# Optimization experiments

Measured on AMD Instinct MI355X. Metric: run time of the kernel, lower is better.

The kernel has to match this reference:

```python
import jax, jax.numpy as jnp
import numpy as np

B, Q, E, NH, L, P = 8, 1024, 256, 8, 4, 4
DH = E // NH
SHAPES = np.array([[128, 128], [64, 64], [32, 32], [16, 16]], dtype=np.int64)
STARTS = np.concatenate([[0], np.cumsum(SHAPES.prod(1))[:-1]]).astype(np.int64)
S_TOTAL = int(SHAPES.prod(1).sum())
EPS = 1e-5


def setup_inputs() -> dict:
    key = jax.random.key(0)
    ks = iter(jax.random.split(key, 40))
    def rn(shp, s=0.02):
        return jax.random.normal(next(ks), shp, jnp.float32) * s
    return {
        "tgt": rn((B, Q, E), 1.0),
        "query_pos": rn((B, Q, E), 1.0),
        "reference_points": jax.random.uniform(next(ks), (B, Q, L, 2), jnp.float32),
        "src": rn((B, S_TOTAL, E), 1.0),
        "spatial_shapes": jnp.asarray(SHAPES),
        "level_start_index": jnp.asarray(STARTS),
        "in_proj_w": rn((3 * E, E)), "in_proj_b": jnp.zeros((3 * E,), jnp.float32),
        "out_proj_w": rn((E, E)), "out_proj_b": jnp.zeros((E,), jnp.float32),
        "norm1_g": jnp.ones((E,), jnp.float32), "norm1_b": jnp.zeros((E,), jnp.float32),
        "off_w": rn((NH * L * P * 2, E)), "off_b": rn((NH * L * P * 2,), 0.5),
        "aw_w": rn((NH * L * P, E)), "aw_b": jnp.zeros((NH * L * P,), jnp.float32),
        "vp_w": rn((E, E)), "vp_b": jnp.zeros((E,), jnp.float32),
        "op_w": rn((E, E)), "op_b": jnp.zeros((E,), jnp.float32),
        "norm2_g": jnp.ones((E,), jnp.float32), "norm2_b": jnp.zeros((E,), jnp.float32),
        "w1": rn((4 * E, E)), "b1": jnp.zeros((4 * E,), jnp.float32),
        "w2": rn((E, 4 * E)), "b2": jnp.zeros((E,), jnp.float32),
        "norm3_g": jnp.ones((E,), jnp.float32), "norm3_b": jnp.zeros((E,), jnp.float32),
    }


def _ln(x, g, b):
    mu = x.mean(-1, keepdims=True)
    var = ((x - mu) ** 2).mean(-1, keepdims=True)
    return (x - mu) * jax.lax.rsqrt(var + EPS) * g + b


def _bilinear(v, loc, Hl, Wl):
    # v: [B,NH,S_l,DH], loc in [0,1]: [B,NH,Q,P,2] -> [B,NH,Q,P,DH]
    # matches torch grid_sample(align_corners=False, padding='zeros')
    x = loc[..., 0] * Wl - 0.5
    y = loc[..., 1] * Hl - 0.5
    x0 = jnp.floor(x)
    y0 = jnp.floor(y)
    wx = (x - x0)[..., None]
    wy = (y - y0)[..., None]
    def g(yi, xi):
        valid = ((xi >= 0) & (xi <= Wl - 1) & (yi >= 0) & (yi <= Hl - 1)).astype(v.dtype)
        idx = (jnp.clip(yi, 0, Hl - 1) * Wl + jnp.clip(xi, 0, Wl - 1)).astype(jnp.int32)
        out = jnp.take_along_axis(v, idx.reshape(B, NH, Q * P, 1), axis=2)
        return out.reshape(B, NH, Q, P, DH) * valid[..., None]
    v00 = g(y0, x0); v01 = g(y0, x0 + 1.0)
    v10 = g(y0 + 1.0, x0); v11 = g(y0 + 1.0, x0 + 1.0)
    return (v00 * (1 - wy) * (1 - wx) + v01 * (1 - wy) * wx
            + v10 * wy * (1 - wx) + v11 * wy * wx)


def _forward(tgt, query_pos, reference_points, src,
             in_proj_w, in_proj_b, out_proj_w, out_proj_b, norm1_g, norm1_b,
             off_w, off_b, aw_w, aw_b, vp_w, vp_b, op_w, op_b,
             norm2_g, norm2_b, w1, b1, w2, b2, norm3_g, norm3_b,
             spatial_shapes, level_start_index):
    shp = np.asarray(spatial_shapes)
    starts = np.asarray(level_start_index)
    # ---- self-attention (q = k = tgt + pos, v = tgt) ----
    qk = tgt + query_pos
    wq, wk, wv = jnp.split(in_proj_w, 3, axis=0)
    bq, bk, bv = jnp.split(in_proj_b, 3, axis=0)
    q = (qk @ wq.T + bq).reshape(B, Q, NH, DH)
    k = (qk @ wk.T + bk).reshape(B, Q, NH, DH)
    v = (tgt @ wv.T + bv).reshape(B, Q, NH, DH)
    scores = jnp.einsum("bqhd,bkhd->bhqk", q, k) / jnp.sqrt(jnp.float32(DH))
    attn = jax.nn.softmax(scores, axis=-1)
    ctx = jnp.einsum("bhqk,bkhd->bqhd", attn, v).reshape(B, Q, E)
    tgt = _ln(tgt + (ctx @ out_proj_w.T + out_proj_b), norm1_g, norm1_b)
    # ---- MSDA cross-attention ----
    query = tgt + query_pos
    value = (src @ vp_w.T + vp_b).reshape(B, S_TOTAL, NH, DH).transpose(0, 2, 1, 3)  # [B,NH,S,DH]
    off = (query @ off_w.T + off_b).reshape(B, Q, NH, L, P, 2)
    aw = jax.nn.softmax((query @ aw_w.T + aw_b).reshape(B, Q, NH, L * P), -1)
    aw = aw.reshape(B, Q, NH, L, P)
    normalizer = jnp.asarray(shp[:, ::-1].copy(), jnp.float32)  # [L,2] = (W,H)
    loc = reference_points[:, :, None, :, None, :] + off / normalizer[None, None, None, :, None, :]
    loc = jnp.transpose(loc, (0, 2, 1, 3, 4, 5))  # [B,NH,Q,L,P,2]
    awt = jnp.transpose(aw, (0, 2, 1, 3, 4))      # [B,NH,Q,L,P]
    out = jnp.zeros((B, NH, Q, DH), jnp.float32)
    for l in range(L):
        Hl, Wl = int(shp[l, 0]), int(shp[l, 1])
        s0 = int(starts[l])
        vl = value[:, :, s0:s0 + Hl * Wl]
        samp = _bilinear(vl, loc[:, :, :, l], Hl, Wl)         # [B,NH,Q,P,DH]
        out = out + (samp * awt[:, :, :, l, :, None]).sum(3)
    ca = out.transpose(0, 2, 1, 3).reshape(B, Q, E) @ op_w.T + op_b
    tgt = _ln(tgt + ca, norm2_g, norm2_b)
    # ---- FFN ----
    h = jax.nn.relu(tgt @ w1.T + b1) @ w2.T + b2
    return _ln(tgt + h, norm3_g, norm3_b)


def reference(tgt, query_pos, reference_points, src, spatial_shapes, level_start_index,
              in_proj_w, in_proj_b, out_proj_w, out_proj_b, norm1_g, norm1_b,
              off_w, off_b, aw_w, aw_b, vp_w, vp_b, op_w, op_b,
              norm2_g, norm2_b, w1, b1, w2, b2, norm3_g, norm3_b):
    return _forward(tgt, query_pos, reference_points, src,
                    in_proj_w, in_proj_b, out_proj_w, out_proj_b, norm1_g, norm1_b,
                    off_w, off_b, aw_w, aw_b, vp_w, vp_b, op_w, op_b,
                    norm2_g, norm2_b, w1, b1, w2, b2, norm3_g, norm3_b,
                    spatial_shapes, level_start_index)
```

## Files before the change

kernel.cpp:

```cpp
#include <hip/hip_runtime.h>
#include <hip/hip_bf16.h>
#include <math.h>

typedef __hip_bfloat16 bf16;
typedef unsigned short ushort_t;

#define BQ 8
#define QLEN 1024
#define EMB 256
#define NHD 8
#define NLVL 4
#define NPT 4
#define DHD 32
#define STOT 21760

typedef short s8v __attribute__((ext_vector_type(8)));
typedef float f4v __attribute__((ext_vector_type(4)));

__device__ __forceinline__ float b2f(bf16 x) { return __bfloat162float(x); }

__device__ __forceinline__ float ldin(const void* p, int bf, size_t i) {
    return bf ? __bfloat162float(((const bf16*)p)[i]) : ((const float*)p)[i];
}

__device__ __forceinline__ float bfraw(unsigned u) {
    union { unsigned i; float f; } c; c.i = u << 16; return c.f;
}

__device__ __forceinline__ unsigned short f2us(float x) {
    bf16 h = __float2bfloat16(x);
    unsigned short u;
    __builtin_memcpy(&u, &h, 2);
    return u;
}

__device__ __forceinline__ void ld4(const void* p, int bf, size_t i, float* o) {
    if (bf) {
        const uint2 u = *(const uint2*)((const ushort_t*)p + i);
        o[0] = bfraw(u.x & 0xffffu); o[1] = bfraw(u.x >> 16);
        o[2] = bfraw(u.y & 0xffffu); o[3] = bfraw(u.y >> 16);
    } else {
        const float4 f = *(const float4*)((const float*)p + i);
        o[0] = f.x; o[1] = f.y; o[2] = f.z; o[3] = f.w;
    }
}

typedef const __attribute__((address_space(1))) unsigned int* gas1_u32;
typedef __attribute__((address_space(3))) unsigned int* las3_u32;
__device__ __forceinline__ void gload_lds16(const void* g, void* l) {
    __builtin_amdgcn_global_load_lds((gas1_u32)g, (las3_u32)l, 16, 0, 0);
}

__global__ void detect_dtype(const unsigned* __restrict__ n1g, int* __restrict__ flag) {
    if (threadIdx.x == 0) flag[0] = (n1g[0] == 0x3F800000u) ? 0 : 1;
}

template <int BN, int KT, int WAVES, bool ARAW, bool RELU, typename CT>
__global__ __launch_bounds__(WAVES * 64) void gemm_wlds(
        const void* __restrict__ A,
        const void* __restrict__ W, int w0,
        const void* __restrict__ bias, int b0,
        CT* __restrict__ C,
        int M, int N,
        const int* __restrict__ dflag) {
    constexpr int T = WAVES * 64;
    constexpr int GPR = KT / 8;
    constexpr int WSLOTS = BN * GPR;
    constexpr int NJ = BN / 16;
    constexpr int KC = KT / 256;
    constexpr int CW = BN < 128 ? BN : 128;
    constexpr int NCH = BN / CW;
    constexpr int JC = CW / 16;
    constexpr int ST_US = (sizeof(CT) == 2) ? (CW + 8) : 2 * (CW + 12);
    constexpr int EPI_US = WAVES * 16 * ST_US;
    constexpr int SMEM_US = (BN * KT) > EPI_US ? (BN * KT) : EPI_US;

    __shared__ __align__(16) ushort_t smem[SMEM_US];

    const int bfm = *dflag;
    const int tid = threadIdx.x;
    const int lane = tid & 63;
    const int wv = tid >> 6;
    const int l15 = lane & 15, lhi = lane >> 4;
    const int n0 = blockIdx.x * BN;
    const int mg = blockIdx.y * (16 * WAVES) + wv * 16;

#pragma unroll
    for (int i = 0; i < WSLOTS / T; ++i) {
        const int s0 = (wv << 6) + T * i;
        const int s = s0 + lane;
        const int n = s / GPR;
        const int gl = s & (GPR - 1);
        const int gg = (gl + GPR - (n & (GPR - 1))) & (GPR - 1);
        const size_t woff = (size_t)(w0 + n0 + n) * KT + gg * 8;
        if (bfm) {
            gload_lds16((const ushort_t*)W + woff, smem + (size_t)s0 * 8);
        } else {
            const float* wf = (const float*)W + woff;
            const float4 f0 = *(const float4*)wf;
            const float4 f1 = *(const float4*)(wf + 4);
            ushort_t t[8] = {f2us(f0.x), f2us(f0.y), f2us(f0.z), f2us(f0.w),
                             f2us(f1.x), f2us(f1.y), f2us(f1.z), f2us(f1.w)};
            *(uint4*)(smem + (size_t)s * 8) = *(uint4*)t;
        }
    }

    auto ldA = [&](int kc, s8v* af) {
#pragma unroll
        for (int kk = 0; kk < 8; ++kk) {
            const size_t ao = (size_t)(mg + l15) * KT + kc * 256 + kk * 32 + lhi * 8;
            if (!ARAW || bfm) {
                af[kk] = *(const s8v*)((const ushort_t*)A + ao);
            } else {
                const float* ap = (const float*)A + ao;
                const float4 f0 = *(const float4*)ap;
                const float4 f1 = *(const float4*)(ap + 4);
                ushort_t t[8] = {f2us(f0.x), f2us(f0.y), f2us(f0.z), f2us(f0.w),
                                 f2us(f1.x), f2us(f1.y), f2us(f1.z), f2us(f1.w)};
                af[kk] = *(const s8v*)t;
            }
        }
    };

    f4v acc[NJ] = {};
    s8v afA[8], afB[8];
    ldA(0, afA);
    __syncthreads();

#pragma unroll
    for (int kc = 0; kc < KC; ++kc) {
        s8v* af = (kc & 1) ? afB : afA;
        s8v* afn = (kc & 1) ? afA : afB;
        if (kc + 1 < KC) ldA(kc + 1, afn);
#pragma unroll
        for (int j = 0; j < NJ; ++j) {
            const int n = j * 16 + l15;
#pragma unroll
            for (int kk = 0; kk < 8; ++kk) {
                const int gg = kc * 32 + kk * 4 + lhi;
                const int gl = (gg + n) & (GPR - 1);
                const s8v b = *(const s8v*)(smem + (size_t)n * KT + gl * 8);
                acc[j] = __builtin_amdgcn_mfma_f32_16x16x32_bf16(af[kk], b, acc[j], 0, 0, 0);
            }
        }
    }
    __syncthreads();

    if constexpr (sizeof(CT) == 2) {
        ushort_t* eb = smem + wv * 16 * ST_US;
#pragma unroll
        for (int c = 0; c < NCH; ++c) {
#pragma unroll
            for (int jj = 0; jj < JC; ++jj) {
                const int j = c * JC + jj;
                const float bv = ldin(bias, bfm, b0 + n0 + j * 16 + l15);
#pragma unroll
                for (int p = 0; p < 4; ++p) {
                    float v = acc[j][p] + bv;
                    if (RELU) v = fmaxf(v, 0.f);
                    eb[(lhi * 4 + p) * ST_US + jj * 16 + l15] = f2us(v);
                }
            }
            asm volatile("s_waitcnt lgkmcnt(0)" ::: "memory");
            __builtin_amdgcn_sched_barrier(0);
            constexpr int GPRow = CW / 8;
            constexpr int RPP = 64 / GPRow;
#pragma unroll
            for (int pass = 0; pass < 16 / RPP; ++pass) {
                const int row = pass * RPP + lane / GPRow;
                const int g = lane % GPRow;
                const uint4 u = *(const uint4*)(eb + row * ST_US + g * 8);
                *(uint4*)((ushort_t*)C + (size_t)(mg + row) * N + n0 + c * CW + g * 8) = u;
            }
            asm volatile("s_waitcnt lgkmcnt(0)" ::: "memory");
            __builtin_amdgcn_sched_barrier(0);
        }
    } else {
        constexpr int ST_F = CW + 12;
        float* ef = (float*)(smem) + wv * 16 * ST_F;
#pragma unroll
        for (int c = 0; c < NCH; ++c) {
#pragma unroll
            for (int jj = 0; jj < JC; ++jj) {
                const int j = c * JC + jj;
                const float bv = ldin(bias, bfm, b0 + n0 + j * 16 + l15);
#pragma unroll
                for (int p = 0; p < 4; ++p) {
                    float v = acc[j][p] + bv;
                    if (RELU) v = fmaxf(v, 0.f);
                    ef[(lhi * 4 + p) * ST_F + jj * 16 + l15] = v;
                }
            }
            asm volatile("s_waitcnt lgkmcnt(0)" ::: "memory");
            __builtin_amdgcn_sched_barrier(0);
            constexpr int GPRow = CW / 4;
            constexpr int RPP = 64 / GPRow;
#pragma unroll
            for (int pass = 0; pass < 16 / RPP; ++pass) {
                const int row = pass * RPP + lane / GPRow;
                const int g = lane % GPRow;
                const float4 u = *(const float4*)(ef + row * ST_F + g * 4);
                *(float4*)((float*)C + (size_t)(mg + row) * N + n0 + c * CW + g * 4) = u;
            }
            asm volatile("s_waitcnt lgkmcnt(0)" ::: "memory");
            __builtin_amdgcn_sched_barrier(0);
        }
    }
}

__global__ void ew_add_bf(const void* __restrict__ a, const void* __restrict__ b,
                          ushort_t* __restrict__ c, int n4, const int* __restrict__ dflag) {
    const int bfm = *dflag;
    const int i = blockIdx.x * 256 + threadIdx.x;
    if (i < n4) {
        float ta[4], tb[4];
        ld4(a, bfm, (size_t)i * 4, ta);
        ld4(b, bfm, (size_t)i * 4, tb);
        uint2 u;
        u.x = (unsigned)f2us(ta[0] + tb[0]) | ((unsigned)f2us(ta[1] + tb[1]) << 16);
        u.y = (unsigned)f2us(ta[2] + tb[2]) | ((unsigned)f2us(ta[3] + tb[3]) << 16);
        *(uint2*)(c + (size_t)i * 4) = u;
    }
}

__global__ __launch_bounds__(256) void attn_mfma(const ushort_t* __restrict__ qkbuf,
                                                 const ushort_t* __restrict__ v,
                                                 ushort_t* __restrict__ ctx) {
    __shared__ ushort_t Ks[64][40];
    __shared__ ushort_t Vt[32][72];
    __shared__ ushort_t Ps[4][16][72];
    const int bh = blockIdx.y;
    const int b = bh >> 3, h = bh & 7;
    const int qt = blockIdx.x;
    const int tid = threadIdx.x;
    const int lane = tid & 63;
    const int wv = tid >> 6;
    const int l15 = lane & 15, quad = lane >> 4;
    const float scale = 0.17677669529663689f;

    const int qbase = (qt << 6) + (wv << 4);
    const s8v qfrag = *(const s8v*)(qkbuf +
        ((size_t)(b * QLEN + qbase + l15)) * 512 + h * DHD + quad * 8);

    const int sk = tid >> 2;
    const int sd = (tid & 3) << 3;

    float m_run[4] = {-1e30f, -1e30f, -1e30f, -1e30f};
    float l_run[4] = {};
    f4v o[2] = {};

    for (int kt = 0; kt < 16; ++kt) {
        __syncthreads();
        const size_t krow = (size_t)(b * QLEN + (kt << 6) + sk);
        *(uint4*)&Ks[sk][sd] = *(const uint4*)(qkbuf + krow * 512 + 256 + h * DHD + sd);
        const uint4 uv = *(const uint4*)(v + krow * 256 + h * DHD + sd);
        ushort_t vt[8];
        *(uint4*)vt = uv;
#pragma unroll
        for (int j = 0; j < 8; ++j) Vt[sd + j][sk] = vt[j];
        __syncthreads();

        f4v s4[4];
#pragma unroll
        for (int kb = 0; kb < 4; ++kb) {
            const s8v kfr = *(const s8v*)&Ks[(kb << 4) + l15][quad * 8];
            s4[kb] = __builtin_amdgcn_mfma_f32_16x16x32_bf16(qfrag, kfr, f4v{}, 0, 0, 0);
        }

        float sc[4][4];
#pragma unroll
        for (int kb = 0; kb < 4; ++kb)
#pragma unroll
            for (int p = 0; p < 4; ++p) sc[kb][p] = s4[kb][p] * scale;
        float mp[4];
#pragma unroll
        for (int p = 0; p < 4; ++p)
            mp[p] = fmaxf(fmaxf(sc[0][p], sc[1][p]), fmaxf(sc[2][p], sc[3][p]));
#pragma unroll
        for (int p = 0; p < 4; ++p) {
            mp[p] = fmaxf(mp[p], __shfl_xor(mp[p], 1, 64));
            mp[p] = fmaxf(mp[p], __shfl_xor(mp[p], 2, 64));
            mp[p] = fmaxf(mp[p], __shfl_xor(mp[p], 4, 64));
            mp[p] = fmaxf(mp[p], __shfl_xor(mp[p], 8, 64));
        }
        float al[4], ls[4] = {};
#pragma unroll
        for (int p = 0; p < 4; ++p) {
            const float mn = fmaxf(m_run[p], mp[p]);
            al[p] = __expf(m_run[p] - mn);
            m_run[p] = mn;
        }
        float pe[4][4];
#pragma unroll
        for (int kb = 0; kb < 4; ++kb)
#pragma unroll
            for (int p = 0; p < 4; ++p) {
                const float e = __expf(sc[kb][p] - m_run[p]);
                pe[kb][p] = e;
                ls[p] += e;
            }
#pragma unroll
        for (int p = 0; p < 4; ++p) {
            ls[p] += __shfl_xor(ls[p], 1, 64);
            ls[p] += __shfl_xor(ls[p], 2, 64);
            ls[p] += __shfl_xor(ls[p], 4, 64);
            ls[p] += __shfl_xor(ls[p], 8, 64);
            l_run[p] = l_run[p] * al[p] + ls[p];
        }
#pragma unroll
        for (int nb = 0; nb < 2; ++nb)
#pragma unroll
            for (int p = 0; p < 4; ++p) o[nb][p] *= al[p];

#pragma unroll
        for (int kb = 0; kb < 4; ++kb)
#pragma unroll
            for (int p = 0; p < 4; ++p)
                Ps[wv][(quad << 2) + p][(kb << 4) + l15] = f2us(pe[kb][p]);

#pragma unroll
        for (int kk = 0; kk < 2; ++kk) {
            const s8v afr = *(const s8v*)&Ps[wv][l15][kk * 32 + quad * 8];
#pragma unroll
            for (int nb = 0; nb < 2; ++nb) {
                const s8v bfr = *(const s8v*)&Vt[nb * 16 + l15][kk * 32 + quad * 8];
                o[nb] = __builtin_amdgcn_mfma_f32_16x16x32_bf16(afr, bfr, o[nb], 0, 0, 0);
            }
        }
    }

#pragma unroll
    for (int p = 0; p < 4; ++p) {
        const float inv = 1.f / l_run[p];
        const size_t row = (size_t)(b * QLEN + qbase + (quad << 2) + p) * EMB + h * DHD;
#pragma unroll
        for (int nb = 0; nb < 2; ++nb)
            ctx[row + nb * 16 + l15] = f2us(o[nb][p] * inv);
    }
}

__global__ __launch_bounds__(256) void ln_kernel(const void* __restrict__ xb,
                                                 const float* __restrict__ xf1,
                                                 const float* __restrict__ xf2,
                                                 const void* __restrict__ g,
                                                 const void* __restrict__ bta,
                                                 float* __restrict__ out_f,
                                                 ushort_t* __restrict__ out_b,
                                                 void* __restrict__ out_d,
                                                 const void* __restrict__ qp,
                                                 ushort_t* __restrict__ out_q,
                                                 const int* __restrict__ dflag) {
    const int bf = *dflag;
    const int row = blockIdx.x * 4 + (threadIdx.x >> 6);
    const int lane = threadIdx.x & 63;
    const size_t base = (size_t)row * EMB + lane * 4;

    float x[4] = {0.f, 0.f, 0.f, 0.f};
    if (xb) {
        float t[4]; ld4(xb, bf, base, t);
#pragma unroll
        for (int j = 0; j < 4; ++j) x[j] += t[j];
    }
    if (xf1) {
        const float4 f = *(const float4*)(xf1 + base);
        x[0] += f.x; x[1] += f.y; x[2] += f.z; x[3] += f.w;
    }
    if (xf2) {
        const float4 f = *(const float4*)(xf2 + base);
        x[0] += f.x; x[1] += f.y; x[2] += f.z; x[3] += f.w;
    }
    float s = x[0] + x[1] + x[2] + x[3];
#pragma unroll
    for (int o = 1; o < 64; o <<= 1) s += __shfl_xor(s, o, 64);
    const float mu = s * (1.f / EMB);
    float dx[4], vs = 0.f;
#pragma unroll
    for (int j = 0; j < 4; ++j) { dx[j] = x[j] - mu; vs += dx[j] * dx[j]; }
#pragma unroll
    for (int o = 1; o < 64; o <<= 1) vs += __shfl_xor(vs, o, 64);
    const float inv = rsqrtf(vs * (1.f / EMB) + 1e-5f);

    float gv[4], bv[4];
    ld4(g, bf, (size_t)lane * 4, gv);
    ld4(bta, bf, (size_t)lane * 4, bv);
    float y[4];
#pragma unroll
    for (int j = 0; j < 4; ++j) y[j] = dx[j] * inv * gv[j] + bv[j];

    if (out_f) *(float4*)(out_f + base) = float4{y[0], y[1], y[2], y[3]};
    if (out_b) {
        uint2 u;
        u.x = (unsigned)f2us(y[0]) | ((unsigned)f2us(y[1]) << 16);
        u.y = (unsigned)f2us(y[2]) | ((unsigned)f2us(y[3]) << 16);
        *(uint2*)(out_b + base) = u;
    }
    if (out_d) {
        if (bf) {
            uint2 u;
            u.x = (unsigned)f2us(y[0]) | ((unsigned)f2us(y[1]) << 16);
            u.y = (unsigned)f2us(y[2]) | ((unsigned)f2us(y[3]) << 16);
            *(uint2*)((ushort_t*)out_d + base) = u;
        } else {
            *(float4*)((float*)out_d + base) = float4{y[0], y[1], y[2], y[3]};
        }
    }
    if (out_q) {
        float q[4]; ld4(qp, bf, base, q);
        uint2 u;
        u.x = (unsigned)f2us(y[0] + q[0]) | ((unsigned)f2us(y[1] + q[1]) << 16);
        u.y = (unsigned)f2us(y[2] + q[2]) | ((unsigned)f2us(y[3] + q[3]) << 16);
        *(uint2*)(out_q + base) = u;
    }
}

__global__ __launch_bounds__(64) void sample_kernel(const float* __restrict__ offb,
                                                    const float* __restrict__ awb,
                                                    const void* __restrict__ refp,
                                                    const ushort_t* __restrict__ value,
                                                    ushort_t* __restrict__ out,
                                                    const int* __restrict__ dflag) {
    const int bf = *dflag;
    const int bid = blockIdx.x;
    const int h = bid & 7;
    const int bq = bid >> 3;
    const int b = bq >> 10;
    const int lane = threadIdx.x;
    const int s_idx = lane >> 2;
    const int dg = lane & 3;
    const int l = s_idx >> 2;

    float logit = awb[(size_t)bq * 128 + h * 16 + s_idx];
    float m = logit;
#pragma unroll
    for (int o = 32; o > 0; o >>= 1) m = fmaxf(m, __shfl_xor(m, o, 64));
    float e = __expf(logit - m);
    float ssum = e;
#pragma unroll
    for (int o = 32; o > 0; o >>= 1) ssum += __shfl_xor(ssum, o, 64);
    const float paw = 4.f * e / ssum;

    const int Wi = 128 >> l;
    const float Wl = (float)Wi, Hl = (float)Wi;
    const int s0 = (l == 0) ? 0 : (l == 1) ? 16384 : (l == 2) ? 20480 : 21504;

    const float rx = ldin(refp, bf, ((size_t)bq * NLVL + l) * 2 + 0);
    const float ry = ldin(refp, bf, ((size_t)bq * NLVL + l) * 2 + 1);
    const float ox = offb[(size_t)bq * 256 + h * 32 + s_idx * 2 + 0];
    const float oy = offb[(size_t)bq * 256 + h * 32 + s_idx * 2 + 1];
    const float x = (rx + ox / Wl) * Wl - 0.5f;
    const float y = (ry + oy / Hl) * Hl - 0.5f;
    const float x0 = floorf(x), y0 = floorf(y);
    const float wx = x - x0, wy = y - y0;

    float acc[8] = {};
    const ushort_t* vbase = value + ((size_t)b * STOT) * EMB + h * DHD + dg * 8;

    auto corner = [&](float yi, float xi, float w) {
        const bool valid = (xi >= 0.f) && (xi <= Wl - 1.f) && (yi >= 0.f) && (yi <= Hl - 1.f);
        const float xc = fminf(fmaxf(xi, 0.f), Wl - 1.f);
        const float yc = fminf(fmaxf(yi, 0.f), Hl - 1.f);
        const int row = s0 + (int)yc * Wi + (int)xc;
        const uint4 u = *(const uint4*)(vbase + (size_t)row * EMB);
        const float wv = valid ? w : 0.f;
        const unsigned ua[4] = {u.x, u.y, u.z, u.w};
#pragma unroll
        for (int j = 0; j < 4; ++j) {
            acc[2 * j + 0] = fmaf(wv, bfraw(ua[j] & 0xffffu), acc[2 * j + 0]);
            acc[2 * j + 1] = fmaf(wv, bfraw(ua[j] >> 16), acc[2 * j + 1]);
        }
    };
    corner(y0, x0, (1.f - wy) * (1.f - wx));
    corner(y0, x0 + 1.f, (1.f - wy) * wx);
    corner(y0 + 1.f, x0, wy * (1.f - wx));
    corner(y0 + 1.f, x0 + 1.f, wy * wx);

#pragma unroll
    for (int j = 0; j < 8; ++j) {
        float vj = acc[j] * paw;
        vj += __shfl_xor(vj, 4, 64);
        vj += __shfl_xor(vj, 8, 64);
        vj += __shfl_xor(vj, 16, 64);
        vj += __shfl_xor(vj, 32, 64);
        acc[j] = vj;
    }
    if (s_idx == 0) {
        ushort_t t[8];
#pragma unroll
        for (int j = 0; j < 8; ++j) t[j] = f2us(acc[j]);
        *(uint4*)(out + (size_t)bq * EMB + h * DHD + dg * 8) = *(uint4*)t;
    }
}

extern "C" void kernel_launch(void* const* d_in, const int* in_sizes, int n_in,
                              void* d_out, int out_size, void* d_ws, size_t ws_size,
                              hipStream_t stream) {
    const void* tgt  = d_in[0];
    const void* qp   = d_in[1];
    const void* refp = d_in[2];
    const void* src  = d_in[3];
    const void* ipw  = d_in[6];
    const void* ipb  = d_in[7];
    const void* oprw = d_in[8];
    const void* oprb = d_in[9];
    const void* n1g  = d_in[10];
    const void* n1b  = d_in[11];
    const void* ofw  = d_in[12];
    const void* ofb  = d_in[13];
    const void* aww  = d_in[14];
    const void* awbv = d_in[15];
    const void* vpw  = d_in[16];
    const void* vpb  = d_in[17];
    const void* opw2 = d_in[18];
    const void* opb2 = d_in[19];
    const void* n2g  = d_in[20];
    const void* n2b  = d_in[21];
    const void* w1   = d_in[22];
    const void* b1   = d_in[23];
    const void* w2   = d_in[24];
    const void* b2   = d_in[25];
    const void* n3g  = d_in[26];
    const void* n3b  = d_in[27];

    const int M = BQ * QLEN;
    const int MS = BQ * STOT;

    char* ws = (char*)d_ws;
    int* dflag = (int*)ws;
    size_t o = 256;
    char* S1 = ws + o; o += (size_t)M * EMB * 2;
    char* S2 = ws + o; o += (size_t)M * 512 * 2;
    char* S3 = ws + o; o += (size_t)M * EMB * 2;
    char* S4 = ws + o; o += (size_t)M * EMB * 2;
    char* S5 = ws + o; o += (size_t)M * EMB * 4;
    char* S6 = ws + o; o += (size_t)M * EMB * 4;
    char* S7 = ws + o; o += (size_t)M * EMB * 4;
    char* S8 = ws + o;

    ushort_t* qk_bf    = (ushort_t*)S1;
    ushort_t* samp_bf  = (ushort_t*)S1;
    ushort_t* qkproj   = (ushort_t*)S2;
    float*    off_f    = (float*)S2;
    ushort_t* vproj    = (ushort_t*)S3;
    ushort_t* qry_bf   = (ushort_t*)S3;
    ushort_t* tgt2_bf  = (ushort_t*)S3;
    ushort_t* ctx_bf   = (ushort_t*)S4;
    float*    awl_f    = (float*)S4;
    float*    bufD     = (float*)S5;
    float*    tgt1_f   = (float*)S6;
    float*    tgt2_f   = (float*)S7;
    ushort_t* value_bf = (ushort_t*)S8;
    ushort_t* h1_bf    = (ushort_t*)S8;

    detect_dtype<<<1, 64, 0, stream>>>((const unsigned*)n1g, dflag);

    ew_add_bf<<<(M * EMB / 4) / 256, 256, 0, stream>>>(tgt, qp, qk_bf, M * EMB / 4, dflag);
    gemm_wlds<64, 256, 4, false, false, ushort_t><<<dim3(8, M / 64), 256, 0, stream>>>(
        qk_bf, ipw, 0, ipb, 0, qkproj, M, 512, dflag);
    gemm_wlds<64, 256, 4, true, false, ushort_t><<<dim3(4, M / 64), 256, 0, stream>>>(
        tgt, ipw, 512, ipb, 512, vproj, M, 256, dflag);
    attn_mfma<<<dim3(16, BQ * NHD), 256, 0, stream>>>(qkproj, vproj, ctx_bf);
    gemm_wlds<64, 256, 4, false, false, float><<<dim3(4, M / 64), 256, 0, stream>>>(
        ctx_bf, oprw, 0, oprb, 0, bufD, M, 256, dflag);
    ln_kernel<<<M / 4, 256, 0, stream>>>(tgt, bufD, nullptr, n1g, n1b,
                                         tgt1_f, nullptr, nullptr, qp, qry_bf, dflag);

    gemm_wlds<64, 256, 4, false, false, float><<<dim3(4, M / 64), 256, 0, stream>>>(
        qry_bf, ofw, 0, ofb, 0, off_f, M, 256, dflag);
    gemm_wlds<64, 256, 4, false, false, float><<<dim3(2, M / 64), 256, 0, stream>>>(
        qry_bf, aww, 0, awbv, 0, awl_f, M, 128, dflag);
    gemm_wlds<256, 256, 16, true, false, ushort_t><<<dim3(1, MS / 256), 1024, 0, stream>>>(
        src, vpw, 0, vpb, 0, value_bf, MS, 256, dflag);
    sample_kernel<<<M * NHD, 64, 0, stream>>>(off_f, awl_f, refp, value_bf, samp_bf, dflag);
    gemm_wlds<64, 256, 4, false, false, float><<<dim3(4, M / 64), 256, 0, stream>>>(
        samp_bf, opw2, 0, opb2, 0, bufD, M, 256, dflag);
    ln_kernel<<<M / 4, 256, 0, stream>>>(nullptr, tgt1_f, bufD, n2g, n2b,
                                         tgt2_f, tgt2_bf, nullptr, nullptr, nullptr, dflag);

    gemm_wlds<64, 256, 4, false, true, ushort_t><<<dim3(16, M / 64), 256, 0, stream>>>(
        tgt2_bf, w1, 0, b1, 0, h1_bf, M, 1024, dflag);
    gemm_wlds<32, 1024, 4, false, false, float><<<dim3(8, M / 64), 256, 0, stream>>>(
        h1_bf, w2, 0, b2, 0, bufD, M, 256, dflag);
    ln_kernel<<<M / 4, 256, 0, stream>>>(nullptr, tgt2_f, bufD, n3g, n3b,
                                         nullptr, nullptr, d_out, nullptr, nullptr, dflag);
}
```

Baseline: 596.5 us.

## Add double-buffered GEMM for value projection, fuse q+pos add, pack sampler blocks

Adds a new double-buffered, swizzled LDS GEMM (128x256 tiles, 8 waves, K-step 32) and uses it for the large src value projection instead of the single-stage full-K kernel. Folds the tgt+query_pos add into the QK projection's A-load, which drops the separate elementwise kernel and its intermediate buffer. Packs four sampling wavefronts per 256-thread block to cut block count. These trade more complex code and extra A loads in the fused GEMM for less launch and memory traffic.

```diff
diff --git a/kernel.cpp b/kernel.cpp
--- a/kernel.cpp
+++ b/kernel.cpp
@@ -55,9 +55,164 @@
     if (threadIdx.x == 0) flag[0] = (n1g[0] == 0x3F800000u) ? 0 : 1;
 }
 
-template <int BN, int KT, int WAVES, bool ARAW, bool RELU, typename CT>
+template <bool ARAW, bool RELU, typename CT, int WR, int WC>
+__global__ __launch_bounds__(64 * WR * WC) void gemm_dbuf(
+        const void* __restrict__ A,
+        const void* __restrict__ W, int w0,
+        const void* __restrict__ bias, int b0,
+        CT* __restrict__ C,
+        int M, int N, int K,
+        const int* __restrict__ dflag) {
+    constexpr int T = 64 * WR * WC;
+    constexpr int NW = WR * WC;
+    constexpr int BM = 64 * WR, BN = 64 * WC;
+    constexpr int ACH = (BM * 4) / T;
+    constexpr int BCH = (BN * 4) / T;
+    constexpr int BUF_US = (BM + BN) * 32;
+    constexpr int EPI_US = NW * 16 * 88;
+    constexpr int SMEM_US = (2 * BUF_US) > EPI_US ? (2 * BUF_US) : EPI_US;
+
+    const int bfm = *dflag;
+    __shared__ __align__(16) ushort_t smem[SMEM_US];
+
+    const int tid = threadIdx.x;
+    const int lane = tid & 63;
+    const int wv = tid >> 6;
+    const int wrow = (wv % WR) << 6;
+    const int wcol = (wv / WR) << 6;
+    const int m0 = blockIdx.x * BM, n0 = blockIdx.y * BN;
+    const int l15 = lane & 15, lhi = lane >> 4;
+    const int swz = (l15 >> 1) & 3;
+
+    f4v acc[4][4] = {};
+
+    auto stage = [&](int k0, int buf) {
+        ushort_t* As = smem + buf * BUF_US;
+        ushort_t* Bs = As + BM * 32;
+#pragma unroll
+        for (int i = 0; i < ACH; ++i) {
+            const int s0 = (wv << 6) + T * i;
+            const int s = s0 + lane;
+            const int r = s >> 2;
+            const int gd = (s & 3) ^ ((r >> 1) & 3);
+            const size_t aoff = (size_t)(m0 + r) * K + k0 + gd * 8;
+            if (!ARAW || bfm) {
+                gload_lds16((const ushort_t*)A + aoff, As + (size_t)s0 * 8);
+            } else {
+                const float* af = (const float*)A + aoff;
+                const float4 f0 = *(const float4*)af;
+                const float4 f1 = *(const float4*)(af + 4);
+                ushort_t t[8] = {f2us(f0.x), f2us(f0.y), f2us(f0.z), f2us(f0.w),
+                                 f2us(f1.x), f2us(f1.y), f2us(f1.z), f2us(f1.w)};
+                *(uint4*)(As + (size_t)s * 8) = *(uint4*)t;
+            }
+        }
+#pragma unroll
+        for (int i = 0; i < BCH; ++i) {
+            const int s0 = (wv << 6) + T * i;
+            const int s = s0 + lane;
+            const int r = s >> 2;
+            const int gd = (s & 3) ^ ((r >> 1) & 3);
+            const size_t woff = (size_t)(w0 + n0 + r) * K + k0 + gd * 8;
+            if (bfm) {
+                gload_lds16((const ushort_t*)W + woff, Bs + (size_t)s0 * 8);
+            } else {
+                const float* wf = (const float*)W + woff;
+                const float4 f0 = *(const float4*)wf;
+                const float4 f1 = *(const float4*)(wf + 4);
+                ushort_t t[8] = {f2us(f0.x), f2us(f0.y), f2us(f0.z), f2us(f0.w),
+                                 f2us(f1.x), f2us(f1.y), f2us(f1.z), f2us(f1.w)};
+                *(uint4*)(Bs + (size_t)s * 8) = *(uint4*)t;
+            }
+        }
+    };
+
+    stage(0, 0);
+    __syncthreads();
+    int cur = 0;
+    for (int k0 = 0; k0 < K; k0 += 32) {
+        if (k0 + 32 < K) stage(k0 + 32, cur ^ 1);
+
+        const ushort_t* As = smem + cur * BUF_US;
+        const ushort_t* Bs = As + BM * 32;
+        s8v afr[4], bfr[4];
+#pragma unroll
+        for (int i = 0; i < 4; ++i)
+            afr[i] = *(const s8v*)(As + (wrow + i * 16 + l15) * 32 + ((lhi ^ swz) << 3));
+#pragma unroll
+        for (int j = 0; j < 4; ++j)
+            bfr[j] = *(const s8v*)(Bs + (wcol + j * 16 + l15) * 32 + ((lhi ^ swz) << 3));
+#pragma unroll
+        for (int i = 0; i < 4; ++i)
+#pragma unroll
+            for (int j = 0; j < 4; ++j)
+                acc[i][j] = __builtin_amdgcn_mfma_f32_16x16x32_bf16(
+                    afr[i], bfr[j], acc[i][j], 0, 0, 0);
+        __syncthreads();
+        cur ^= 1;
+    }
+
+    if (sizeof(CT) == 2) {
+        ushort_t* eb = smem + wv * 16 * 88;
+#pragma unroll
+        for (int i = 0; i < 4; ++i) {
+#pragma unroll
+            for (int j = 0; j < 4; ++j) {
+                const int n = n0 + wcol + j * 16 + l15;
+                const float bv = ldin(bias, bfm, b0 + n);
+#pragma unroll
+                for (int p = 0; p < 4; ++p) {
+                    float v = acc[i][j][p] + bv;
+                    if (RELU) v = fmaxf(v, 0.f);
+                    eb[(lhi * 4 + p) * 88 + j * 16 + l15] = f2us(v);
+                }
+            }
+#pragma unroll
+            for (int pass = 0; pass < 2; ++pass) {
+                const int row = pass * 8 + (lane >> 3);
+                const int g = lane & 7;
+                const uint4 u = *(const uint4*)(eb + row * 88 + g * 8);
+                const int m = m0 + wrow + i * 16 + row;
+                const int n = n0 + wcol + g * 8;
+                *(uint4*)((ushort_t*)C + (size_t)m * N + n) = u;
+            }
+        }
+    } else {
+        float* ef = (float*)smem + wv * 16 * 44;
+#pragma unroll
+        for (int i = 0; i < 4; ++i) {
+#pragma unroll
+            for (int jp = 0; jp < 2; ++jp) {
+#pragma unroll
+                for (int j2 = 0; j2 < 2; ++j2) {
+                    const int j = jp * 2 + j2;
+                    const int n = n0 + wcol + j * 16 + l15;
+                    const float bv = ldin(bias, bfm, b0 + n);
+#pragma unroll
+                    for (int p = 0; p < 4; ++p) {
+                        float v = acc[i][j][p] + bv;
+                        if (RELU) v = fmaxf(v, 0.f);
+                        ef[(lhi * 4 + p) * 44 + j2 * 16 + l15] = v;
+                    }
+                }
+#pragma unroll
+                for (int pass = 0; pass < 2; ++pass) {
+                    const int row = pass * 8 + (lane >> 3);
+                    const int g = lane & 7;
+                    const float4 u = *(const float4*)(ef + row * 44 + g * 4);
+                    const int m = m0 + wrow + i * 16 + row;
+                    const int n = n0 + wcol + jp * 32 + g * 4;
+                    *(float4*)((float*)C + (size_t)m * N + n) = u;
+                }
+            }
+        }
+    }
+}
+
+template <int BN, int KT, int WAVES, bool ARAW, bool ADD2, bool RELU, typename CT>
 __global__ __launch_bounds__(WAVES * 64) void gemm_wlds(
         const void* __restrict__ A,
+        const void* __restrict__ A2,
         const void* __restrict__ W, int w0,
         const void* __restrict__ bias, int b0,
         CT* __restrict__ C,
@@ -109,7 +264,15 @@
 #pragma unroll
         for (int kk = 0; kk < 8; ++kk) {
             const size_t ao = (size_t)(mg + l15) * KT + kc * 256 + kk * 32 + lhi * 8;
-            if (!ARAW || bfm) {
+            if constexpr (ADD2) {
+                float a[8], b[8];
+                ld4(A, bfm, ao, a);  ld4(A, bfm, ao + 4, a + 4);
+                ld4(A2, bfm, ao, b); ld4(A2, bfm, ao + 4, b + 4);
+                ushort_t t[8];
+#pragma unroll
+                for (int j = 0; j < 8; ++j) t[j] = f2us(a[j] + b[j]);
+                af[kk] = *(const s8v*)t;
+            } else if (!ARAW || bfm) {
                 af[kk] = *(const s8v*)((const ushort_t*)A + ao);
             } else {
                 const float* ap = (const float*)A + ao;
@@ -205,21 +368,6 @@
             asm volatile("s_waitcnt lgkmcnt(0)" ::: "memory");
             __builtin_amdgcn_sched_barrier(0);
         }
-    }
-}
-
-__global__ void ew_add_bf(const void* __restrict__ a, const void* __restrict__ b,
-                          ushort_t* __restrict__ c, int n4, const int* __restrict__ dflag) {
-    const int bfm = *dflag;
-    const int i = blockIdx.x * 256 + threadIdx.x;
-    if (i < n4) {
-        float ta[4], tb[4];
-        ld4(a, bfm, (size_t)i * 4, ta);
-        ld4(b, bfm, (size_t)i * 4, tb);
-        uint2 u;
-        u.x = (unsigned)f2us(ta[0] + tb[0]) | ((unsigned)f2us(ta[1] + tb[1]) << 16);
-        u.y = (unsigned)f2us(ta[2] + tb[2]) | ((unsigned)f2us(ta[3] + tb[3]) << 16);
-        *(uint2*)(c + (size_t)i * 4) = u;
     }
 }
 
@@ -413,18 +561,18 @@
     }
 }
 
-__global__ __launch_bounds__(64) void sample_kernel(const float* __restrict__ offb,
-                                                    const float* __restrict__ awb,
-                                                    const void* __restrict__ refp,
-                                                    const ushort_t* __restrict__ value,
-                                                    ushort_t* __restrict__ out,
-                                                    const int* __restrict__ dflag) {
+__global__ __launch_bounds__(256) void sample_kernel(const float* __restrict__ offb,
+                                                     const float* __restrict__ awb,
+                                                     const void* __restrict__ refp,
+                                                     const ushort_t* __restrict__ value,
+                                                     ushort_t* __restrict__ out,
+                                                     const int* __restrict__ dflag) {
     const int bf = *dflag;
-    const int bid = blockIdx.x;
+    const int bid = blockIdx.x * 4 + (threadIdx.x >> 6);
     const int h = bid & 7;
     const int bq = bid >> 3;
     const int b = bq >> 10;
-    const int lane = threadIdx.x;
+    const int lane = threadIdx.x & 63;
     const int s_idx = lane >> 2;
     const int dg = lane & 3;
     const int l = s_idx >> 2;
@@ -536,7 +684,6 @@
     char* S7 = ws + o; o += (size_t)M * EMB * 4;
     char* S8 = ws + o;
 
-    ushort_t* qk_bf    = (ushort_t*)S1;
     ushort_t* samp_bf  = (ushort_t*)S1;
     ushort_t* qkproj   = (ushort_t*)S2;
     float*    off_f    = (float*)S2;
@@ -553,33 +700,32 @@
 
     detect_dtype<<<1, 64, 0, stream>>>((const unsigned*)n1g, dflag);
 
-    ew_add_bf<<<(M * EMB / 4) / 256, 256, 0, stream>>>(tgt, qp, qk_bf, M * EMB / 4, dflag);
-    gemm_wlds<64, 256, 4, false, false, ushort_t><<<dim3(8, M / 64), 256, 0, stream>>>(
-        qk_bf, ipw, 0, ipb, 0, qkproj, M, 512, dflag);
-    gemm_wlds<64, 256, 4, true, false, ushort_t><<<dim3(4, M / 64), 256, 0, stream>>>(
-        tgt, ipw, 512, ipb, 512, vproj, M, 256, dflag);
+    gemm_wlds<64, 256, 4, true, true, false, ushort_t><<<dim3(8, M / 64), 256, 0, stream>>>(
+        tgt, qp, ipw, 0, ipb, 0, qkproj, M, 512, dflag);
+    gemm_wlds<64, 256, 4, true, false, false, ushort_t><<<dim3(4, M / 64), 256, 0, stream>>>(
+        tgt, nullptr, ipw, 512, ipb, 512, vproj, M, 256, dflag);
     attn_mfma<<<dim3(16, BQ * NHD), 256, 0, stream>>>(qkproj, vproj, ctx_bf);
-    gemm_wlds<64, 256, 4, false, false, float><<<dim3(4, M / 64), 256, 0, stream>>>(
-        ctx_bf, oprw, 0, oprb, 0, bufD, M, 256, dflag);
+    gemm_wlds<64, 256, 4, false, false, false, float><<<dim3(4, M / 64), 256, 0, stream>>>(
+        ctx_bf, nullptr, oprw, 0, oprb, 0, bufD, M, 256, dflag);
     ln_kernel<<<M / 4, 256, 0, stream>>>(tgt, bufD, nullptr, n1g, n1b,
                                          tgt1_f, nullptr, nullptr, qp, qry_bf, dflag);
 
-    gemm_wlds<64, 256, 4, false, false, float><<<dim3(4, M / 64), 256, 0, stream>>>(
-        qry_bf, ofw, 0, ofb, 0, off_f, M, 256, dflag);
-    gemm_wlds<64, 256, 4, false, false, float><<<dim3(2, M / 64), 256, 0, stream>>>(
-        qry_bf, aww, 0, awbv, 0, awl_f, M, 128, dflag);
-    gemm_wlds<256, 256, 16, true, false, ushort_t><<<dim3(1, MS / 256), 1024, 0, stream>>>(
-        src, vpw, 0, vpb, 0, value_bf, MS, 256, dflag);
-    sample_kernel<<<M * NHD, 64, 0, stream>>>(off_f, awl_f, refp, value_bf, samp_bf, dflag);
-    gemm_wlds<64, 256, 4, false, false, float><<<dim3(4, M / 64), 256, 0, stream>>>(
-        samp_bf, opw2, 0, opb2, 0, bufD, M, 256, dflag);
+    gemm_wlds<64, 256, 4, false, false, false, float><<<dim3(4, M / 64), 256, 0, stream>>>(
+        qry_bf, nullptr, ofw, 0, ofb, 0, off_f, M, 256, dflag);
+    gemm_wlds<64, 256, 4, false, false, false, float><<<dim3(2, M / 64), 256, 0, stream>>>(
+        qry_bf, nullptr, aww, 0, awbv, 0, awl_f, M, 128, dflag);
+    gemm_dbuf<true, false, ushort_t, 2, 4><<<dim3(MS / 128, 1), 512, 0, stream>>>(
+        src, vpw, 0, vpb, 0, value_bf, MS, 256, 256, dflag);
+    sample_kernel<<<(M * NHD) / 4, 256, 0, stream>>>(off_f, awl_f, refp, value_bf, samp_bf, dflag);
+    gemm_wlds<64, 256, 4, false, false, false, float><<<dim3(4, M / 64), 256, 0, stream>>>(
+        samp_bf, nullptr, opw2, 0, opb2, 0, bufD, M, 256, dflag);
     ln_kernel<<<M / 4, 256, 0, stream>>>(nullptr, tgt1_f, bufD, n2g, n2b,
                                          tgt2_f, tgt2_bf, nullptr, nullptr, nullptr, dflag);
 
-    gemm_wlds<64, 256, 4, false, true, ushort_t><<<dim3(16, M / 64), 256, 0, stream>>>(
-        tgt2_bf, w1, 0, b1, 0, h1_bf, M, 1024, dflag);
-    gemm_wlds<32, 1024, 4, false, false, float><<<dim3(8, M / 64), 256, 0, stream>>>(
-        h1_bf, w2, 0, b2, 0, bufD, M, 256, dflag);
+    gemm_wlds<64, 256, 4, false, false, true, ushort_t><<<dim3(16, M / 64), 256, 0, stream>>>(
+        tgt2_bf, nullptr, w1, 0, b1, 0, h1_bf, M, 1024, dflag);
+    gemm_wlds<32, 1024, 4, false, false, false, float><<<dim3(8, M / 64), 256, 0, stream>>>(
+        h1_bf, nullptr, w2, 0, b2, 0, bufD, M, 256, dflag);
     ln_kernel<<<M / 4, 256, 0, stream>>>(nullptr, tgt2_f, bufD, n3g, n3b,
                                          nullptr, nullptr, d_out, nullptr, nullptr, dflag);
 }
```

Result: no change. 604.5 us (+1.3%).
